# Kernel tuning notes

Hardware: AMD Instinct MI355X
Metric: run time of the kernel (lower is better)

The kernel has to match this reference:

```python
import jax, jax.numpy as jnp
import numpy as np

EMBED_DIM = 1024
NUM_HEADS = 16
HEAD_DIM = EMBED_DIM // NUM_HEADS
B, S = 2, 2048
NEG = -1e20


def setup_inputs() -> dict:
    key = jax.random.key(0)
    ks = jax.random.split(key, 8)
    scale = 0.02
    return {
        "query": jax.random.normal(ks[0], (B, S, EMBED_DIM), jnp.float32),
        "keys": jax.random.normal(ks[1], (B, S, EMBED_DIM), jnp.float32),
        "values": jax.random.normal(ks[2], (B, S, EMBED_DIM), jnp.float32),
        "mask": jax.random.randint(ks[3], (1, 1, S, S), 0, 2, jnp.int32),
        "Wq": jax.random.normal(ks[4], (EMBED_DIM, EMBED_DIM), jnp.float32) * scale,
        "Wk": jax.random.normal(ks[5], (EMBED_DIM, EMBED_DIM), jnp.float32) * scale,
        "Wv": jax.random.normal(ks[6], (EMBED_DIM, EMBED_DIM), jnp.float32) * scale,
        "Wo": jax.random.normal(ks[7], (EMBED_DIM, EMBED_DIM), jnp.float32) * scale,
        "bo": jnp.zeros((EMBED_DIM,), jnp.float32),
    }


def reference(query, keys, values, mask, Wq, Wk, Wv, Wo, bo):
    N, Lq, _ = query.shape
    Lk = keys.shape[1]
    # torch nn.Linear: y = x @ W.T  (bias=False for Q/K/V)
    Q = (query @ Wq.T).reshape(N, Lq, NUM_HEADS, HEAD_DIM)
    K = (keys @ Wk.T).reshape(N, Lk, NUM_HEADS, HEAD_DIM)
    V = (values @ Wv.T).reshape(N, Lk, NUM_HEADS, HEAD_DIM)
    # NOTE: source scales by sqrt(embed_dim), not sqrt(head_dim) — kept faithful.
    energy = jnp.einsum("nqhd,nkhd->nhqk", Q, K) / jnp.sqrt(
        jnp.asarray(EMBED_DIM, Q.dtype)
    )
    energy = jnp.where(mask == 0, jnp.asarray(NEG, energy.dtype), energy)
    attention = jax.nn.softmax(energy, axis=3)
    out = jnp.einsum("nhqk,nkhd->nqhd", attention, V).reshape(N, Lq, EMBED_DIM)
    return out @ Wo.T + bo
```

## Files before the change

kernel.cpp:

```cpp
#include <hip/hip_runtime.h>
#include <stdint.h>

typedef __bf16 bf16;
typedef __bf16 bf16x4 __attribute__((ext_vector_type(4)));
typedef __bf16 bf16x8 __attribute__((ext_vector_type(8)));
typedef float f32x4 __attribute__((ext_vector_type(4)));

#define MFMA16(a, b, c) __builtin_amdgcn_mfma_f32_16x16x32_bf16((a), (b), (c), 0, 0, 0)

__device__ __forceinline__ void gload16(const bf16* g, bf16* l) {
    __builtin_amdgcn_global_load_lds(
        (const __attribute__((address_space(1))) void*)g,
        (__attribute__((address_space(3))) void*)l, 16, 0, 0);
}

__global__ __launch_bounds__(256) void cvt_kernel(
    const float* __restrict__ q, const float* __restrict__ k, const float* __restrict__ v,
    const float* __restrict__ wq, const float* __restrict__ wk,
    const float* __restrict__ wv, const float* __restrict__ wo,
    bf16* __restrict__ qb, bf16* __restrict__ kb, bf16* __restrict__ vb,
    bf16* __restrict__ wqb, bf16* __restrict__ wkb, bf16* __restrict__ wvb,
    bf16* __restrict__ wob)
{
    int z = blockIdx.z;
    const float* src; bf16* dst; int n;
    switch (z) {
        case 0:  src = q;  dst = qb;  n = 4194304; break;
        case 1:  src = k;  dst = kb;  n = 4194304; break;
        case 2:  src = v;  dst = vb;  n = 4194304; break;
        case 3:  src = wq; dst = wqb; n = 1048576; break;
        case 4:  src = wk; dst = wkb; n = 1048576; break;
        case 5:  src = wv; dst = wvb; n = 1048576; break;
        default: src = wo; dst = wob; n = 1048576; break;
    }
    int i = (blockIdx.x * 256 + threadIdx.x) * 8;
    if (i >= n) return;
    float4 f0 = *(const float4*)(src + i);
    float4 f1 = *(const float4*)(src + i + 4);
    bf16x8 o;
    o[0] = (bf16)f0.x; o[1] = (bf16)f0.y; o[2] = (bf16)f0.z; o[3] = (bf16)f0.w;
    o[4] = (bf16)f1.x; o[5] = (bf16)f1.y; o[6] = (bf16)f1.z; o[7] = (bf16)f1.w;
    *(bf16x8*)(dst + i) = o;
}

__global__ __launch_bounds__(256) void maskpack_kernel(
    const int* __restrict__ mask, unsigned long long* __restrict__ maskb)
{
    int gid  = blockIdx.x * 256 + threadIdx.x;
    int word = gid >> 6;
    int lane = gid & 63;
    int row = word >> 5, wc = word & 31;
    int mv = mask[row * 2048 + wc * 64 + lane];
    unsigned long long bits = __ballot(mv != 0);
    if (lane == 0) maskb[word] = bits;
}

template <int OUTMODE, int MT>
__global__ __launch_bounds__(256) void gemm_kernel(
    const bf16* __restrict__ A0, const bf16* __restrict__ A1, const bf16* __restrict__ A2,
    const bf16* __restrict__ B0, const bf16* __restrict__ B1, const bf16* __restrict__ B2,
    bf16* __restrict__ C0, bf16* __restrict__ C1, bf16* __restrict__ C2,
    const float* __restrict__ bias, float* __restrict__ outf)
{
    constexpr int MI = (MT == 128) ? 4 : 2;

    const int z = blockIdx.z;
    const bf16* A = (z == 0) ? A0 : (z == 1) ? A1 : A2;
    const bf16* B = (z == 0) ? B0 : (z == 1) ? B1 : B2;

    __shared__ bf16 At[MT * 32];
    __shared__ bf16 Bt[128 * 32];

    const int tid  = threadIdx.x;
    const int lane = tid & 63;
    const int wave = tid >> 6;
    const int quad = lane >> 4;
    const int l16  = lane & 15;
    const int wm = (wave >> 1) * (MT / 2);
    const int wn = (wave & 1) * 64;
    const int m0 = blockIdx.y * MT;
    const int n0 = blockIdx.x * 128;

    const int lrow = lane >> 2;
    const int lcol = (lane & 3) * 8;

    f32x4 acc[MI][4] = {};

    const bf16* Ag = A + (size_t)(m0 + lrow) * 1024 + lcol;
    const bf16* Bg = B + (size_t)(n0 + lrow) * 1024 + lcol;

    for (int k0 = 0; k0 < 1024; k0 += 32) {
        __syncthreads();
        if constexpr (MT == 128) {
#pragma unroll
            for (int j = 0; j < 2; ++j)
                gload16(Ag + (size_t)(wave * 32 + j * 16) * 1024 + k0,
                        At + (wave * 32 + j * 16) * 32);
        } else {
            gload16(Ag + (size_t)(wave * 16) * 1024 + k0, At + (wave * 16) * 32);
        }
#pragma unroll
        for (int j = 0; j < 2; ++j)
            gload16(Bg + (size_t)(wave * 32 + j * 16) * 1024 + k0,
                    Bt + (wave * 32 + j * 16) * 32);
        __syncthreads();

        bf16x8 af[MI], bg[4];
#pragma unroll
        for (int i = 0; i < MI; ++i)
            af[i] = *(const bf16x8*)(At + (wm + i * 16 + l16) * 32 + quad * 8);
#pragma unroll
        for (int j = 0; j < 4; ++j)
            bg[j] = *(const bf16x8*)(Bt + (wn + j * 16 + l16) * 32 + quad * 8);
#pragma unroll
        for (int i = 0; i < MI; ++i)
#pragma unroll
            for (int j = 0; j < 4; ++j)
                acc[i][j] = MFMA16(af[i], bg[j], acc[i][j]);
    }

    if constexpr (OUTMODE == 0) {
        bf16* C = (z == 0) ? C0 : (z == 1) ? C1 : C2;
        const float cs = (z == 0) ? 0.03125f : 1.0f;
#pragma unroll
        for (int i = 0; i < MI; ++i)
#pragma unroll
            for (int j = 0; j < 4; ++j) {
                int row = m0 + wm + i * 16 + quad * 4;
                int col = n0 + wn + j * 16 + l16;
#pragma unroll
                for (int r = 0; r < 4; ++r)
                    C[(row + r) * 1024 + col] = (bf16)(acc[i][j][r] * cs);
            }
    } else {
#pragma unroll
        for (int j = 0; j < 4; ++j) {
            int col = n0 + wn + j * 16 + l16;
            float bj = bias[col];
#pragma unroll
            for (int i = 0; i < MI; ++i) {
                int row = m0 + wm + i * 16 + quad * 4;
#pragma unroll
                for (int r = 0; r < 4; ++r)
                    outf[(row + r) * 1024 + col] = acc[i][j][r] + bj;
            }
        }
    }
}

__global__ __launch_bounds__(256) void transpose_kernel(const bf16* __restrict__ V,
                                                        bf16* __restrict__ Vt)
{
    __shared__ bf16 t[64][72];
    const int tid = threadIdx.x;
    const int b  = blockIdx.z;
    const int s0 = blockIdx.x * 64;
    const int d0 = blockIdx.y * 64;
#pragma unroll
    for (int c = 0; c < 2; ++c) {
        int qq = c * 256 + tid;
        int row = qq >> 3, col = (qq & 7) * 8;
        *(uint4*)(&t[row][col]) =
            *(const uint4*)(V + (size_t)(b * 2048 + s0 + row) * 1024 + d0 + col);
    }
    __syncthreads();
#pragma unroll
    for (int c = 0; c < 2; ++c) {
        int qq = c * 256 + tid;
        int drow = qq >> 3, scol = (qq & 7) * 8;
        bf16x8 o;
#pragma unroll
        for (int j = 0; j < 8; ++j) o[j] = t[scol + j][drow];
        *(bf16x8*)(Vt + (size_t)(b * 1024 + d0 + drow) * 2048 + s0 + scol) = o;
    }
}

__global__ __launch_bounds__(256) void flash_kernel(
    const bf16* __restrict__ Q, const bf16* __restrict__ K, const bf16* __restrict__ Vt,
    const unsigned long long* __restrict__ maskb, bf16* __restrict__ O)
{
    __shared__ bf16 Kl[64 * 72];
    __shared__ bf16 Vl[64 * 72];
    __shared__ bf16 Pl[4][16 * 72];

    const int tid  = threadIdx.x;
    const int lane = tid & 63;
    const int wave = tid >> 6;
    const int quad = lane >> 4;
    const int l16  = lane & 15;
    const int b  = blockIdx.z;
    const int h  = blockIdx.y;
    const int q0 = blockIdx.x * 64;
    const int qrow = q0 + wave * 16;

    const bf16* Qb = Q + (size_t)(b * 2048 + qrow + l16) * 1024 + h * 64 + quad * 8;
    bf16x8 qf0 = *(const bf16x8*)(Qb);
    bf16x8 qf1 = *(const bf16x8*)(Qb + 32);

    bf16x8 ones;
#pragma unroll
    for (int j = 0; j < 8; ++j) ones[j] = (bf16)1.0f;

    f32x4 acc[4] = {};
    f32x4 lacc = {};

    const int srow = tid >> 3;
    const int scol = (tid & 7) * 8;
    const bf16* Kg = K + (size_t)(b * 2048 + srow) * 1024 + h * 64 + scol;
    bf16*       Kw = Kl + srow * 72 + scol;
    const bf16* Vg = Vt + (size_t)((b * 16 + h) * 64 + srow) * 2048 + scol;
    bf16*       Vw = Vl + srow * 72 + scol;
    const unsigned long long* Mg = maskb + (size_t)(qrow + l16) * 32;

    bf16* Pw = Pl[wave];

    for (int kt = 0; kt < 2048; kt += 64) {
        uint4 kv0 = *(const uint4*)(Kg + (size_t)kt * 1024);
        uint4 kv1 = *(const uint4*)(Kg + (size_t)(kt + 32) * 1024);
        uint4 vv0 = *(const uint4*)(Vg + kt);
        uint4 vv1 = *(const uint4*)(Vg + 32 * 2048 + kt);
        unsigned long long mw = Mg[kt >> 6];

        __syncthreads();
        *(uint4*)(Kw)           = kv0;
        *(uint4*)(Kw + 32 * 72) = kv1;
        *(uint4*)(Vw)           = vv0;
        *(uint4*)(Vw + 32 * 72) = vv1;
        __syncthreads();

#pragma unroll
        for (int kf = 0; kf < 4; ++kf) {
            bf16x8 ka0 = *(const bf16x8*)(Kl + (kf * 16 + l16) * 72 + quad * 8);
            bf16x8 ka1 = *(const bf16x8*)(Kl + (kf * 16 + l16) * 72 + 32 + quad * 8);
            f32x4 s = {};
            s = MFMA16(ka0, qf0, s);
            s = MFMA16(ka1, qf1, s);
            bf16x4 pv;
#pragma unroll
            for (int r = 0; r < 4; ++r) {
                bool keep = (mw >> (kf * 16 + quad * 4 + r)) & 1ULL;
                float e = __expf(s[r]);
                pv[r] = keep ? (bf16)e : (bf16)0.0f;
            }
            *(bf16x4*)(Pw + l16 * 72 + kf * 16 + quad * 4) = pv;
        }

        bf16x8 pa0 = *(const bf16x8*)(Pw + l16 * 72 + quad * 8);
        bf16x8 pa1 = *(const bf16x8*)(Pw + l16 * 72 + 32 + quad * 8);
#pragma unroll
        for (int nc = 0; nc < 4; ++nc) {
            bf16x8 vb0 = *(const bf16x8*)(Vl + (nc * 16 + l16) * 72 + quad * 8);
            bf16x8 vb1 = *(const bf16x8*)(Vl + (nc * 16 + l16) * 72 + 32 + quad * 8);
            acc[nc] = MFMA16(pa0, vb0, acc[nc]);
            acc[nc] = MFMA16(pa1, vb1, acc[nc]);
        }
        lacc = MFMA16(pa0, ones, lacc);
        lacc = MFMA16(pa1, ones, lacc);
    }

    const int orow = b * 2048 + qrow + quad * 4;
#pragma unroll
    for (int r = 0; r < 4; ++r) {
        float inv = 1.0f / lacc[r];
#pragma unroll
        for (int nc = 0; nc < 4; ++nc)
            O[(size_t)(orow + r) * 1024 + h * 64 + nc * 16 + l16] =
                (bf16)(acc[nc][r] * inv);
    }
}

extern "C" void kernel_launch(void* const* d_in, const int* in_sizes, int n_in,
                              void* d_out, int out_size, void* d_ws, size_t ws_size,
                              hipStream_t stream)
{
    const float* q  = (const float*)d_in[0];
    const float* k  = (const float*)d_in[1];
    const float* v  = (const float*)d_in[2];
    const int* mask = (const int*)d_in[3];
    const float* wq = (const float*)d_in[4];
    const float* wk = (const float*)d_in[5];
    const float* wv = (const float*)d_in[6];
    const float* wo = (const float*)d_in[7];
    const float* bo = (const float*)d_in[8];
    float* out = (float*)d_out;

    char* p = (char*)d_ws;
    auto alloc = [&](size_t bytes) {
        char* r = p;
        p += (bytes + 255) & ~(size_t)255;
        return r;
    };
    const size_t SB = (size_t)4096 * 1024 * 2;
    const size_t WB = (size_t)1024 * 1024 * 2;
    bf16* qb  = (bf16*)alloc(SB);
    bf16* kb  = (bf16*)alloc(SB);
    bf16* vb  = (bf16*)alloc(SB);
    bf16* wqb = (bf16*)alloc(WB);
    bf16* wkb = (bf16*)alloc(WB);
    bf16* wvb = (bf16*)alloc(WB);
    bf16* wob = (bf16*)alloc(WB);
    bf16* Qp  = (bf16*)alloc(SB);
    bf16* Kp  = (bf16*)alloc(SB);
    bf16* Vp  = (bf16*)alloc(SB);
    bf16* Vtp = (bf16*)alloc(SB);
    bf16* Ob  = (bf16*)alloc(SB);
    unsigned long long* maskb = (unsigned long long*)alloc(2048 * 32 * 8);

    cvt_kernel<<<dim3(2048, 1, 7), 256, 0, stream>>>(
        q, k, v, wq, wk, wv, wo, qb, kb, vb, wqb, wkb, wvb, wob);

    maskpack_kernel<<<dim3(16384), 256, 0, stream>>>(mask, maskb);

    gemm_kernel<0, 128><<<dim3(8, 32, 3), 256, 0, stream>>>(
        qb, kb, vb, wqb, wkb, wvb, Qp, Kp, Vp, nullptr, nullptr);

    transpose_kernel<<<dim3(32, 16, 2), 256, 0, stream>>>(Vp, Vtp);

    flash_kernel<<<dim3(32, 16, 2), 256, 0, stream>>>(Qp, Kp, Vtp, maskb, Ob);

    gemm_kernel<1, 64><<<dim3(8, 64, 1), 256, 0, stream>>>(
        Ob, nullptr, nullptr, wob, nullptr, nullptr,
        nullptr, nullptr, nullptr, bo, out);
}
```

Baseline: 260.7 us.

## Rework flash attention to 32x32 MFMA with 128-query tiles and direct LDS loads

The flash kernel now runs 32x32x16 bf16 MFMAs and gives each wave 32 query rows, so a block covers 128 queries and the grid is halved. K and V tiles reuse across twice as many queries, which cuts global traffic per query. K/V staging switches from register round-trips to global_load_lds with an XOR-swizzled, unpadded layout meant to avoid bank conflicts. In exchange the kernel uses more registers (f32x16 accumulators) and launches fewer blocks, which may lower occupancy.

```diff
diff --git a/kernel.cpp b/kernel.cpp
--- a/kernel.cpp
+++ b/kernel.cpp
@@ -5,8 +5,10 @@
 typedef __bf16 bf16x4 __attribute__((ext_vector_type(4)));
 typedef __bf16 bf16x8 __attribute__((ext_vector_type(8)));
 typedef float f32x4 __attribute__((ext_vector_type(4)));
+typedef float f32x16 __attribute__((ext_vector_type(16)));
 
 #define MFMA16(a, b, c) __builtin_amdgcn_mfma_f32_16x16x32_bf16((a), (b), (c), 0, 0, 0)
+#define MFMA32(a, b, c) __builtin_amdgcn_mfma_f32_32x32x16_bf16((a), (b), (c), 0, 0, 0)
 
 __device__ __forceinline__ void gload16(const bf16* g, bf16* l) {
     __builtin_amdgcn_global_load_lds(
@@ -179,94 +181,102 @@
     const bf16* __restrict__ Q, const bf16* __restrict__ K, const bf16* __restrict__ Vt,
     const unsigned long long* __restrict__ maskb, bf16* __restrict__ O)
 {
-    __shared__ bf16 Kl[64 * 72];
-    __shared__ bf16 Vl[64 * 72];
-    __shared__ bf16 Pl[4][16 * 72];
+    __shared__ bf16 Kl[64 * 64];
+    __shared__ bf16 Vl[64 * 64];
+    __shared__ bf16 Pl[128 * 72];
 
     const int tid  = threadIdx.x;
     const int lane = tid & 63;
     const int wave = tid >> 6;
-    const int quad = lane >> 4;
-    const int l16  = lane & 15;
+    const int l32  = lane & 31;
+    const int hl   = lane >> 5;
+    const int l7   = lane & 7;
     const int b  = blockIdx.z;
     const int h  = blockIdx.y;
-    const int q0 = blockIdx.x * 64;
-    const int qrow = q0 + wave * 16;
-
-    const bf16* Qb = Q + (size_t)(b * 2048 + qrow + l16) * 1024 + h * 64 + quad * 8;
-    bf16x8 qf0 = *(const bf16x8*)(Qb);
-    bf16x8 qf1 = *(const bf16x8*)(Qb + 32);
+    const int q0 = blockIdx.x * 128;
+    const int qt = q0 + wave * 32;
+
+    const bf16* Qb = Q + (size_t)(b * 2048 + qt + l32) * 1024 + h * 64 + hl * 8;
+    bf16x8 qf[4];
+#pragma unroll
+    for (int ks = 0; ks < 4; ++ks) qf[ks] = *(const bf16x8*)(Qb + ks * 16);
 
     bf16x8 ones;
 #pragma unroll
     for (int j = 0; j < 8; ++j) ones[j] = (bf16)1.0f;
 
-    f32x4 acc[4] = {};
-    f32x4 lacc = {};
-
-    const int srow = tid >> 3;
-    const int scol = (tid & 7) * 8;
-    const bf16* Kg = K + (size_t)(b * 2048 + srow) * 1024 + h * 64 + scol;
-    bf16*       Kw = Kl + srow * 72 + scol;
-    const bf16* Vg = Vt + (size_t)((b * 16 + h) * 64 + srow) * 2048 + scol;
-    bf16*       Vw = Vl + srow * 72 + scol;
-    const unsigned long long* Mg = maskb + (size_t)(qrow + l16) * 32;
-
-    bf16* Pw = Pl[wave];
+    f32x16 acc[2] = {};
+    f32x16 lacc = {};
+
+    const int dmarow = lane >> 3;
+    const int dmacol = (l7 ^ dmarow) * 8;
+    const bf16* Kg = K + (size_t)(b * 2048 + wave * 16 + dmarow) * 1024 + h * 64 + dmacol;
+    const bf16* Vg = Vt + (size_t)((b * 16 + h) * 64 + wave * 16 + dmarow) * 2048 + dmacol;
+    bf16* Kw = Kl + (wave * 16) * 64;
+    bf16* Vw = Vl + (wave * 16) * 64;
+    const unsigned long long* Mg = maskb + (size_t)(qt + l32) * 32;
+
+    bf16* Pq = Pl + (wave * 32 + l32) * 72;
 
     for (int kt = 0; kt < 2048; kt += 64) {
-        uint4 kv0 = *(const uint4*)(Kg + (size_t)kt * 1024);
-        uint4 kv1 = *(const uint4*)(Kg + (size_t)(kt + 32) * 1024);
-        uint4 vv0 = *(const uint4*)(Vg + kt);
-        uint4 vv1 = *(const uint4*)(Vg + 32 * 2048 + kt);
         unsigned long long mw = Mg[kt >> 6];
-
         __syncthreads();
-        *(uint4*)(Kw)           = kv0;
-        *(uint4*)(Kw + 32 * 72) = kv1;
-        *(uint4*)(Vw)           = vv0;
-        *(uint4*)(Vw + 32 * 72) = vv1;
+        gload16(Kg + (size_t)kt * 1024,       Kw);
+        gload16(Kg + (size_t)(kt + 8) * 1024, Kw + 8 * 64);
+        gload16(Vg + kt,                      Vw);
+        gload16(Vg + kt + 8 * 2048,           Vw + 8 * 64);
         __syncthreads();
 
 #pragma unroll
-        for (int kf = 0; kf < 4; ++kf) {
-            bf16x8 ka0 = *(const bf16x8*)(Kl + (kf * 16 + l16) * 72 + quad * 8);
-            bf16x8 ka1 = *(const bf16x8*)(Kl + (kf * 16 + l16) * 72 + 32 + quad * 8);
-            f32x4 s = {};
-            s = MFMA16(ka0, qf0, s);
-            s = MFMA16(ka1, qf1, s);
-            bf16x4 pv;
-#pragma unroll
-            for (int r = 0; r < 4; ++r) {
-                bool keep = (mw >> (kf * 16 + quad * 4 + r)) & 1ULL;
-                float e = __expf(s[r]);
-                pv[r] = keep ? (bf16)e : (bf16)0.0f;
-            }
-            *(bf16x4*)(Pw + l16 * 72 + kf * 16 + quad * 4) = pv;
+        for (int t = 0; t < 2; ++t) {
+            f32x16 s = {};
+#pragma unroll
+            for (int ks = 0; ks < 4; ++ks) {
+                bf16x8 ka = *(const bf16x8*)(Kl + (t * 32 + l32) * 64 +
+                                             (((ks * 2 + hl) ^ l7) * 8));
+                s = MFMA32(ka, qf[ks], s);
+            }
+            unsigned long long mwt = mw >> (t * 32 + 4 * hl);
+#pragma unroll
+            for (int g = 0; g < 4; ++g) {
+                bf16x4 pv;
+#pragma unroll
+                for (int r = 0; r < 4; ++r) {
+                    bool keep = (mwt >> (8 * g + r)) & 1ULL;
+                    float e = __expf(s[g * 4 + r]);
+                    pv[r] = keep ? (bf16)e : (bf16)0.0f;
+                }
+                *(bf16x4*)(Pq + t * 32 + 4 * hl + 8 * g) = pv;
+            }
         }
 
-        bf16x8 pa0 = *(const bf16x8*)(Pw + l16 * 72 + quad * 8);
-        bf16x8 pa1 = *(const bf16x8*)(Pw + l16 * 72 + 32 + quad * 8);
-#pragma unroll
-        for (int nc = 0; nc < 4; ++nc) {
-            bf16x8 vb0 = *(const bf16x8*)(Vl + (nc * 16 + l16) * 72 + quad * 8);
-            bf16x8 vb1 = *(const bf16x8*)(Vl + (nc * 16 + l16) * 72 + 32 + quad * 8);
-            acc[nc] = MFMA16(pa0, vb0, acc[nc]);
-            acc[nc] = MFMA16(pa1, vb1, acc[nc]);
+        bf16x8 pa[4];
+#pragma unroll
+        for (int ks = 0; ks < 4; ++ks)
+            pa[ks] = *(const bf16x8*)(Pq + ks * 16 + hl * 8);
+#pragma unroll
+        for (int dt = 0; dt < 2; ++dt)
+#pragma unroll
+            for (int ks = 0; ks < 4; ++ks) {
+                bf16x8 vb = *(const bf16x8*)(Vl + (dt * 32 + l32) * 64 +
+                                             (((ks * 2 + hl) ^ l7) * 8));
+                acc[dt] = MFMA32(pa[ks], vb, acc[dt]);
+            }
+#pragma unroll
+        for (int ks = 0; ks < 4; ++ks)
+            lacc = MFMA32(pa[ks], ones, lacc);
+    }
+
+    const size_t obase = (size_t)(b * 2048 + qt) * 1024 + h * 64;
+#pragma unroll
+    for (int g = 0; g < 4; ++g)
+#pragma unroll
+        for (int r = 0; r < 4; ++r) {
+            int qr = 4 * hl + 8 * g + r;
+            float inv = 1.0f / lacc[g * 4 + r];
+            O[obase + (size_t)qr * 1024 + l32]      = (bf16)(acc[0][g * 4 + r] * inv);
+            O[obase + (size_t)qr * 1024 + 32 + l32] = (bf16)(acc[1][g * 4 + r] * inv);
         }
-        lacc = MFMA16(pa0, ones, lacc);
-        lacc = MFMA16(pa1, ones, lacc);
-    }
-
-    const int orow = b * 2048 + qrow + quad * 4;
-#pragma unroll
-    for (int r = 0; r < 4; ++r) {
-        float inv = 1.0f / lacc[r];
-#pragma unroll
-        for (int nc = 0; nc < 4; ++nc)
-            O[(size_t)(orow + r) * 1024 + h * 64 + nc * 16 + l16] =
-                (bf16)(acc[nc][r] * inv);
-    }
 }
 
 extern "C" void kernel_launch(void* const* d_in, const int* in_sizes, int n_in,
@@ -316,7 +326,7 @@
 
     transpose_kernel<<<dim3(32, 16, 2), 256, 0, stream>>>(Vp, Vtp);
 
-    flash_kernel<<<dim3(32, 16, 2), 256, 0, stream>>>(Qp, Kp, Vtp, maskb, Ob);
+    flash_kernel<<<dim3(16, 16, 2), 256, 0, stream>>>(Qp, Kp, Vtp, maskb, Ob);
 
     gemm_kernel<1, 64><<<dim3(8, 64, 1), 256, 0, stream>>>(
         Ob, nullptr, nullptr, wob, nullptr, nullptr,
```

New measurement: 255.3 us. -2.0%, faster.
